# Kernel tuning notes

Measured on AMD Instinct MI355X. Metric: run time of the kernel, lower is better.

Reference implementation:

```python
import jax, jax.numpy as jnp
import numpy as np

N_ATOM, N_TOKEN = 1024, 256
C_S, C_Z, C_ATOM, C_ATOM_PAIR = 384, 128, 128, 16
EPS = 1e-5


def _layer_norm(x, w, b):
    m = jnp.mean(x, axis=-1, keepdims=True)
    v = jnp.mean(jnp.square(x - m), axis=-1, keepdims=True)
    return (x - m) * jax.lax.rsqrt(v + EPS) * w + b


def setup_inputs() -> dict:
    key = jax.random.key(0)
    ks = jax.random.split(key, 12)
    # one-hot atom -> token map (each atom belongs to exactly one token)
    tok_idx = jnp.sort(jax.random.randint(ks[0], (N_ATOM,), 0, N_TOKEN))
    a2t = jax.nn.one_hot(tok_idx, N_TOKEN, dtype=jnp.float32)  # [n_atom, n_token]
    return {
        "atom_to_token_index": a2t,
        "cl": jax.random.normal(ks[1], (N_ATOM, C_ATOM), jnp.float32),
        "plm": jax.random.normal(ks[2], (N_ATOM, N_ATOM, C_ATOM_PAIR), jnp.float32),
        "ql": jax.random.normal(ks[3], (N_ATOM, C_ATOM), jnp.float32),
        "s_trunk": jax.random.normal(ks[4], (N_TOKEN, C_S), jnp.float32),
        "zij": jax.random.normal(ks[5], (N_TOKEN, N_TOKEN, C_Z), jnp.float32),
        "rl": jax.random.normal(ks[6], (N_ATOM, 3), jnp.float32),
        "ln_s_w": jnp.ones((C_S,), jnp.float32),
        "ln_s_b": jnp.zeros((C_S,), jnp.float32),
        "W_s": jax.random.normal(ks[7], (C_S, C_ATOM), jnp.float32) / np.sqrt(C_S),
        "ln_z_w": jnp.ones((C_Z,), jnp.float32),
        "ln_z_b": jnp.zeros((C_Z,), jnp.float32),
        "W_z": jax.random.normal(ks[8], (C_Z, C_ATOM_PAIR), jnp.float32) / np.sqrt(C_Z),
        "W_r": jax.random.normal(ks[9], (3, C_ATOM), jnp.float32) / np.sqrt(3.0),
    }


def reference(atom_to_token_index, cl, plm, ql, s_trunk, zij, rl,
              ln_s_w, ln_s_b, W_s, ln_z_w, ln_z_b, W_z, W_r):
    a2t = atom_to_token_index  # one-hot [n_atom, n_token]
    # cl += Linear_s(LN_s(sum_t s_trunk[t] * a2t[a,t]))  (token->atom broadcast)
    s_atom = jnp.einsum('tc,at->ac', s_trunk, a2t)  # [n_atom, c_s]
    cl = cl + _layer_norm(s_atom, ln_s_w, ln_s_b) @ W_s
    # plm += Linear_z(LN_z(sum_{t,m} zij[t,m] * a2t[a,t] * a2t[b,m]))
    z_at = jnp.einsum('tmc,at->amc', zij, a2t)      # [n_atom, n_token, c_z]
    z_ab = jnp.einsum('amc,bm->abc', z_at, a2t)     # [n_atom, n_atom, c_z]
    plm = plm + _layer_norm(z_ab, ln_z_w, ln_z_b) @ W_z
    # ql += Linear_r(rl)
    ql = ql + rl @ W_r
    return (cl, plm, ql)
```

## Files before the change

### kernel.cpp

```cpp
#include <hip/hip_runtime.h>
#include <hip/hip_bf16.h>

#define NA 1024
#define NT 256
#define CS 384
#define CZ 128
#define CA 128
#define CP 16

typedef __attribute__((ext_vector_type(8))) short short8;
typedef __attribute__((ext_vector_type(4))) float f32x4;

__device__ __forceinline__ float bfu(unsigned short v){ return __uint_as_float(((unsigned)v) << 16); }
__device__ __forceinline__ unsigned short f2bf(float f){
  unsigned u = __float_as_uint(f);
  return (unsigned short)((u + 0x7fffu + ((u >> 16) & 1u)) >> 16);
}
__device__ __forceinline__ unsigned pack2(float lo, float hi){
  return (unsigned)f2bf(lo) | ((unsigned)f2bf(hi) << 16);
}

__device__ __forceinline__ int lbound(const unsigned short* tokL, int key){
  int lo = 0, hi = NA;
  while (lo < hi) { int mid = (lo + hi) >> 1; if ((int)tokL[mid] < key) lo = mid + 1; else hi = mid; }
  return lo;
}

__global__ __launch_bounds__(256) void prep_kernel(
    const float* __restrict__ a2t,
    const float* __restrict__ s_trunk,
    const float* __restrict__ lnsw,
    const float* __restrict__ lnsb,
    const float* __restrict__ Ws,
    unsigned short* __restrict__ tok16,
    unsigned short* __restrict__ ytok)
{
  __shared__ float redS[4], redQ[4];
  __shared__ float lnbuf[CS];
  __shared__ float part[CA];

  const int blk  = blockIdx.x;
  const int tid  = threadIdx.x;
  const int lane = tid & 63;
  const int wv   = tid >> 6;

  if (blk < 256) {
    int a = blk * 4 + wv;
    float4 u = ((const float4*)(a2t + (size_t)a * NT))[lane];
    bool hit = (u.x != 0.f) | (u.y != 0.f) | (u.z != 0.f) | (u.w != 0.f);
    unsigned long long m = __ballot(hit);
    int fl = __ffsll(m) - 1;
    if (lane == fl) {
      int t = lane * 4;
      if (u.x != 0.f)      {  }
      else if (u.y != 0.f) t += 1;
      else if (u.z != 0.f) t += 2;
      else                 t += 3;
      tok16[a] = (unsigned short)t;
    }
  } else {
    int tk = blk - 256;
    float f0 = 0.f, f1 = 0.f;
    if (tid < 192) {
      float2 v = ((const float2*)(s_trunk + (size_t)tk * CS))[tid];
      f0 = v.x; f1 = v.y;
    }
    float s = f0 + f1;
    float q = f0 * f0 + f1 * f1;
    #pragma unroll
    for (int m = 1; m < 64; m <<= 1) { s += __shfl_xor(s, m); q += __shfl_xor(q, m); }
    if (lane == 0) { redS[wv] = s; redQ[wv] = q; }
    __syncthreads();
    if (tid == 0) {
      float S = redS[0] + redS[1] + redS[2] + redS[3];
      float Q = redQ[0] + redQ[1] + redQ[2] + redQ[3];
      float mean = S * (1.f / 384.f);
      float var  = Q * (1.f / 384.f) - mean * mean;
      redS[0] = mean;
      redQ[0] = rsqrtf(var + 1e-5f);
    }
    __syncthreads();
    float mean = redS[0], rstd = redQ[0];
    if (tid < 192) {
      float2 w2 = ((const float2*)lnsw)[tid];
      float2 b2 = ((const float2*)lnsb)[tid];
      lnbuf[2 * tid]     = fmaf((f0 - mean) * rstd, w2.x, b2.x);
      lnbuf[2 * tid + 1] = fmaf((f1 - mean) * rstd, w2.y, b2.y);
    }
    __syncthreads();
    int j = tid & 127, half = tid >> 7;
    float acc = 0.f;
    int c0 = half * 192;
    #pragma unroll 8
    for (int c = c0; c < c0 + 192; ++c)
      acc = fmaf(lnbuf[c], Ws[(size_t)c * CA + j], acc);
    if (half) part[j] = acc;
    __syncthreads();
    if (!half) ytok[(size_t)tk * CA + j] = f2bf(acc + part[j]);
  }
}

__global__ __launch_bounds__(256) void main_kernel(
    const float* __restrict__ cl,
    const float* __restrict__ plm,
    const float* __restrict__ ql,
    const float* __restrict__ rl,
    const float* __restrict__ Wr,
    const float* __restrict__ zij,
    const float* __restrict__ lnzw,
    const float* __restrict__ lnzb,
    const float* __restrict__ Wz,
    const unsigned short* __restrict__ tok16,
    const unsigned short* __restrict__ ytok,
    float* __restrict__ out)
{
  const int blk = blockIdx.x;
  const int tid = threadIdx.x;

  if (blk < 2048) {
    __shared__ unsigned short tokL[NA];
    __shared__ __align__(16) unsigned short ubuf[4 * 16 * 136];
    unsigned short* stage = ubuf;
    float* wlds = (float*)ubuf;

    const int lane = tid & 63;
    const int wv   = tid >> 6;
    const int t    = blk >> 3;
    const int m0   = ((blk >> 1) & 3) << 6;
    const int slot = blk & 1;

    ((uint2*)tokL)[tid] = ((const uint2*)tok16)[tid];
    __syncthreads();

    int s = lbound(tokL, t);
    int e = lbound(tokL, t + 1);
    if (s + slot >= e) return;
    int S = lbound(tokL, m0);
    int E = lbound(tokL, m0 + 64);
    if (S == E) return;

    {
      int r = lane >> 2, q = lane & 3;
      int mrow = m0 + wv * 16 + r;
      const float4* zp = (const float4*)(zij + ((size_t)t * NT + mrow) * CZ + q * 32);
      float x[32];
      float sm = 0.f, ss = 0.f;
      #pragma unroll
      for (int i = 0; i < 8; ++i) {
        float4 v = zp[i];
        x[4 * i]     = v.x; x[4 * i + 1] = v.y;
        x[4 * i + 2] = v.z; x[4 * i + 3] = v.w;
        sm += (v.x + v.y) + (v.z + v.w);
        ss = fmaf(v.x, v.x, ss); ss = fmaf(v.y, v.y, ss);
        ss = fmaf(v.z, v.z, ss); ss = fmaf(v.w, v.w, ss);
      }
      sm += __shfl_xor(sm, 1); sm += __shfl_xor(sm, 2);
      ss += __shfl_xor(ss, 1); ss += __shfl_xor(ss, 2);
      float mean = sm * (1.f / 128.f);
      float var  = ss * (1.f / 128.f) - mean * mean;
      float rstd = rsqrtf(var + 1e-5f);
      unsigned short* st = stage + wv * 2176 + r * 136 + q * 32;
      const float4* lwp = (const float4*)(lnzw + q * 32);
      const float4* lbp = (const float4*)(lnzb + q * 32);
      #pragma unroll
      for (int i = 0; i < 4; ++i) {
        float4 lw0 = lwp[2 * i], lw1 = lwp[2 * i + 1];
        float4 lb0 = lbp[2 * i], lb1 = lbp[2 * i + 1];
        int c = i * 8;
        unsigned o0 = pack2(fmaf((x[c]     - mean) * rstd, lw0.x, lb0.x),
                            fmaf((x[c + 1] - mean) * rstd, lw0.y, lb0.y));
        unsigned o1 = pack2(fmaf((x[c + 2] - mean) * rstd, lw0.z, lb0.z),
                            fmaf((x[c + 3] - mean) * rstd, lw0.w, lb0.w));
        unsigned o2 = pack2(fmaf((x[c + 4] - mean) * rstd, lw1.x, lb1.x),
                            fmaf((x[c + 5] - mean) * rstd, lw1.y, lb1.y));
        unsigned o3 = pack2(fmaf((x[c + 6] - mean) * rstd, lw1.z, lb1.z),
                            fmaf((x[c + 7] - mean) * rstd, lw1.w, lb1.w));
        uint4 ov; ov.x = o0; ov.y = o1; ov.z = o2; ov.w = o3;
        ((uint4*)st)[i] = ov;
      }
      __syncthreads();
      int h = lane >> 4, lm = lane & 15;
      short8 bfrag[4];
      #pragma unroll
      for (int kk = 0; kk < 4; ++kk)
        #pragma unroll
        for (int jj = 0; jj < 8; ++jj)
          bfrag[kk][jj] = (short)f2bf(Wz[(size_t)(kk * 32 + h * 8 + jj) * CP + lm]);
      const unsigned short* sb = stage + wv * 2176;
      short8 af[4];
      #pragma unroll
      for (int kk = 0; kk < 4; ++kk)
        af[kk] = *(const short8*)(sb + lm * 136 + kk * 32 + h * 8);
      f32x4 acc = {0.f, 0.f, 0.f, 0.f};
      #pragma unroll
      for (int kk = 0; kk < 4; ++kk)
        acc = __builtin_amdgcn_mfma_f32_16x16x32_bf16(af[kk], bfrag[kk], acc, 0, 0, 0);
      __syncthreads();
      #pragma unroll
      for (int jj = 0; jj < 4; ++jj)
        wlds[(wv * 16 + h * 4 + jj) * 16 + lm] = acc[jj];
    }
    __syncthreads();

    const float4* plm4 = (const float4*)plm;
    float4* out4 = (float4*)(out + (size_t)NA * CA);
    const int ntask = (E - S) * 4;
    for (int a = s + slot; a < e; a += 2) {
      size_t rowbase = ((size_t)a << 10);
      for (int base = 0; base < ntask; base += 1024) {
        float4 pv[4], wv4[4];
        size_t idx4[4];
        bool act[4];
        #pragma unroll
        for (int j = 0; j < 4; ++j) {
          int task = base + j * 256 + tid;
          act[j] = (task < ntask);
          int tt = act[j] ? task : 0;
          int b = S + (tt >> 2), quar = tt & 3;
          int m = ((int)tokL[b] - m0) & 63;
          idx4[j] = (rowbase + b) * 4 + quar;
          wv4[j] = *(const float4*)(wlds + m * 16 + quar * 4);
          pv[j]  = plm4[idx4[j]];
        }
        #pragma unroll
        for (int j = 0; j < 4; ++j) {
          if (act[j]) {
            float4 ov;
            ov.x = pv[j].x + wv4[j].x; ov.y = pv[j].y + wv4[j].y;
            ov.z = pv[j].z + wv4[j].z; ov.w = pv[j].w + wv4[j].w;
            out4[idx4[j]] = ov;
          }
        }
      }
    }
  } else if (blk < 2560) {
    int idx = (blk - 2048) * 256 + tid;
    int a = idx >> 7, j = idx & 127;
    int ta = (int)tok16[a] & 255;
    out[idx] = cl[idx] + bfu(ytok[(size_t)ta * CA + j]);
  } else {
    int idx = (blk - 2560) * 256 + tid;
    int a = idx >> 7, j = idx & 127;
    float r0 = rl[a * 3 + 0], r1 = rl[a * 3 + 1], r2 = rl[a * 3 + 2];
    float v = ql[idx];
    v = fmaf(r0, Wr[j], v);
    v = fmaf(r1, Wr[CA + j], v);
    v = fmaf(r2, Wr[2 * CA + j], v);
    out[(size_t)NA * CA + (size_t)NA * NA * CP + idx] = v;
  }
}

extern "C" void kernel_launch(void* const* d_in, const int* in_sizes, int n_in,
                              void* d_out, int out_size, void* d_ws, size_t ws_size,
                              hipStream_t stream) {
  const float* a2t     = (const float*)d_in[0];
  const float* cl      = (const float*)d_in[1];
  const float* plm     = (const float*)d_in[2];
  const float* ql      = (const float*)d_in[3];
  const float* s_trunk = (const float*)d_in[4];
  const float* zij     = (const float*)d_in[5];
  const float* rl      = (const float*)d_in[6];
  const float* lnsw    = (const float*)d_in[7];
  const float* lnsb    = (const float*)d_in[8];
  const float* Ws      = (const float*)d_in[9];
  const float* lnzw    = (const float*)d_in[10];
  const float* lnzb    = (const float*)d_in[11];
  const float* Wz      = (const float*)d_in[12];
  const float* Wr      = (const float*)d_in[13];
  float* out = (float*)d_out;

  unsigned short* tok16 = (unsigned short*)d_ws;
  unsigned short* ytok  = (unsigned short*)d_ws + NA;

  prep_kernel<<<512, 256, 0, stream>>>(a2t, s_trunk, lnsw, lnsb, Ws, tok16, ytok);
  main_kernel<<<3072, 256, 0, stream>>>(cl, plm, ql, rl, Wr, zij, lnzw, lnzb, Wz,
                                        tok16, ytok, out);
}
```

Measured before the change: 213.5 us.

## Precompute token-pair LN+projection table, then stream plm with gathered adds

Adds a path that applies LayerNorm and the W_z projection once per token pair (256x256) and stores the result as a bf16 table in workspace. A separate streaming kernel then gathers from that table by atom token indices and adds it to plm, so the LN and matmul are no longer recomputed per atom pair. The old path remains as a fallback when the workspace is too small. The cost is an extra 2 MB table write and read and one more kernel stage, plus bf16 rounding of the projected values.

Result: no change. 210.2 us (-1.5%).

```diff
diff --git a/kernel.cpp b/kernel.cpp
--- a/kernel.cpp
+++ b/kernel.cpp
@@ -10,7 +10,10 @@
 
 typedef __attribute__((ext_vector_type(8))) short short8;
 typedef __attribute__((ext_vector_type(4))) float f32x4;
-
+typedef __attribute__((ext_vector_type(4))) unsigned int u32x4;
+
+__device__ __forceinline__ float bflo(unsigned u){ return __uint_as_float(u << 16); }
+__device__ __forceinline__ float bfhi(unsigned u){ return __uint_as_float(u & 0xffff0000u); }
 __device__ __forceinline__ float bfu(unsigned short v){ return __uint_as_float(((unsigned)v) << 16); }
 __device__ __forceinline__ unsigned short f2bf(float f){
   unsigned u = __float_as_uint(f);
@@ -24,6 +27,201 @@
   int lo = 0, hi = NA;
   while (lo < hi) { int mid = (lo + hi) >> 1; if ((int)tokL[mid] < key) lo = mid + 1; else hi = mid; }
   return lo;
+}
+
+
+__global__ __launch_bounds__(256) void prep_full_kernel(
+    const float* __restrict__ a2t,
+    const float* __restrict__ s_trunk,
+    const float* __restrict__ lnsw,
+    const float* __restrict__ lnsb,
+    const float* __restrict__ Ws,
+    const float* __restrict__ zij,
+    const float* __restrict__ lnzw,
+    const float* __restrict__ lnzb,
+    const float* __restrict__ Wz,
+    unsigned short* __restrict__ tok16,
+    unsigned short* __restrict__ ytok,
+    unsigned short* __restrict__ wtm)
+{
+  __shared__ float redS[4], redQ[4];
+  __shared__ float lnbuf[CS];
+  __shared__ float part[CA];
+  __shared__ __align__(16) unsigned short stage[4 * 16 * 136];
+
+  const int blk  = blockIdx.x;
+  const int tid  = threadIdx.x;
+  const int lane = tid & 63;
+  const int wv   = tid >> 6;
+
+  if (blk < 256) {
+    int a = blk * 4 + wv;
+    float4 u = ((const float4*)(a2t + (size_t)a * NT))[lane];
+    bool hit = (u.x != 0.f) | (u.y != 0.f) | (u.z != 0.f) | (u.w != 0.f);
+    unsigned long long m = __ballot(hit);
+    int fl = __ffsll(m) - 1;
+    if (lane == fl) {
+      int t = lane * 4;
+      if (u.x != 0.f)      { }
+      else if (u.y != 0.f) t += 1;
+      else if (u.z != 0.f) t += 2;
+      else                 t += 3;
+      tok16[a] = (unsigned short)t;
+    }
+  } else if (blk < 512) {
+    int tk = blk - 256;
+    float f0 = 0.f, f1 = 0.f;
+    if (tid < 192) {
+      float2 v = ((const float2*)(s_trunk + (size_t)tk * CS))[tid];
+      f0 = v.x; f1 = v.y;
+    }
+    float s = f0 + f1;
+    float q = f0 * f0 + f1 * f1;
+    #pragma unroll
+    for (int m = 1; m < 64; m <<= 1) { s += __shfl_xor(s, m); q += __shfl_xor(q, m); }
+    if (lane == 0) { redS[wv] = s; redQ[wv] = q; }
+    __syncthreads();
+    if (tid == 0) {
+      float S = redS[0] + redS[1] + redS[2] + redS[3];
+      float Q = redQ[0] + redQ[1] + redQ[2] + redQ[3];
+      float mean = S * (1.f / 384.f);
+      float var  = Q * (1.f / 384.f) - mean * mean;
+      redS[0] = mean;
+      redQ[0] = rsqrtf(var + 1e-5f);
+    }
+    __syncthreads();
+    float mean = redS[0], rstd = redQ[0];
+    if (tid < 192) {
+      float2 w2 = ((const float2*)lnsw)[tid];
+      float2 b2 = ((const float2*)lnsb)[tid];
+      lnbuf[2 * tid]     = fmaf((f0 - mean) * rstd, w2.x, b2.x);
+      lnbuf[2 * tid + 1] = fmaf((f1 - mean) * rstd, w2.y, b2.y);
+    }
+    __syncthreads();
+    int j = tid & 127, half = tid >> 7;
+    float acc = 0.f;
+    int c0 = half * 192;
+    #pragma unroll 8
+    for (int c = c0; c < c0 + 192; ++c)
+      acc = fmaf(lnbuf[c], Ws[(size_t)c * CA + j], acc);
+    if (half) part[j] = acc;
+    __syncthreads();
+    if (!half) ytok[(size_t)tk * CA + j] = f2bf(acc + part[j]);
+  } else {
+    int cb = blk - 512;
+    int r = lane >> 2, q = lane & 3;
+    int rowbase = cb * 64 + wv * 16;
+    const float4* zp = (const float4*)(zij + (size_t)(rowbase + r) * CZ + q * 32);
+    float x[32];
+    float sm = 0.f, ss = 0.f;
+    #pragma unroll
+    for (int i = 0; i < 8; ++i) {
+      float4 v = zp[i];
+      x[4 * i]     = v.x; x[4 * i + 1] = v.y;
+      x[4 * i + 2] = v.z; x[4 * i + 3] = v.w;
+      sm += (v.x + v.y) + (v.z + v.w);
+      ss = fmaf(v.x, v.x, ss); ss = fmaf(v.y, v.y, ss);
+      ss = fmaf(v.z, v.z, ss); ss = fmaf(v.w, v.w, ss);
+    }
+    sm += __shfl_xor(sm, 1); sm += __shfl_xor(sm, 2);
+    ss += __shfl_xor(ss, 1); ss += __shfl_xor(ss, 2);
+    float mean = sm * (1.f / 128.f);
+    float var  = ss * (1.f / 128.f) - mean * mean;
+    float rstd = rsqrtf(var + 1e-5f);
+    unsigned short* st = stage + wv * 2176 + r * 136 + q * 32;
+    const float4* lwp = (const float4*)(lnzw + q * 32);
+    const float4* lbp = (const float4*)(lnzb + q * 32);
+    #pragma unroll
+    for (int i = 0; i < 4; ++i) {
+      float4 lw0 = lwp[2 * i], lw1 = lwp[2 * i + 1];
+      float4 lb0 = lbp[2 * i], lb1 = lbp[2 * i + 1];
+      int c = i * 8;
+      unsigned o0 = pack2(fmaf((x[c]     - mean) * rstd, lw0.x, lb0.x),
+                          fmaf((x[c + 1] - mean) * rstd, lw0.y, lb0.y));
+      unsigned o1 = pack2(fmaf((x[c + 2] - mean) * rstd, lw0.z, lb0.z),
+                          fmaf((x[c + 3] - mean) * rstd, lw0.w, lb0.w));
+      unsigned o2 = pack2(fmaf((x[c + 4] - mean) * rstd, lw1.x, lb1.x),
+                          fmaf((x[c + 5] - mean) * rstd, lw1.y, lb1.y));
+      unsigned o3 = pack2(fmaf((x[c + 6] - mean) * rstd, lw1.z, lb1.z),
+                          fmaf((x[c + 7] - mean) * rstd, lw1.w, lb1.w));
+      uint4 ov; ov.x = o0; ov.y = o1; ov.z = o2; ov.w = o3;
+      ((uint4*)st)[i] = ov;
+    }
+    __syncthreads();
+    int h = lane >> 4, lm = lane & 15;
+    short8 bfrag[4];
+    #pragma unroll
+    for (int kk = 0; kk < 4; ++kk)
+      #pragma unroll
+      for (int jj = 0; jj < 8; ++jj)
+        bfrag[kk][jj] = (short)f2bf(Wz[(size_t)(kk * 32 + h * 8 + jj) * CP + lm]);
+    const unsigned short* sb = stage + wv * 2176;
+    f32x4 acc = {0.f, 0.f, 0.f, 0.f};
+    #pragma unroll
+    for (int kk = 0; kk < 4; ++kk) {
+      short8 af = *(const short8*)(sb + lm * 136 + kk * 32 + h * 8);
+      acc = __builtin_amdgcn_mfma_f32_16x16x32_bf16(af, bfrag[kk], acc, 0, 0, 0);
+    }
+    #pragma unroll
+    for (int jj = 0; jj < 4; ++jj)
+      wtm[(size_t)(rowbase + h * 4 + jj) * CP + lm] = f2bf(acc[jj]);
+  }
+}
+
+__global__ __launch_bounds__(256) void stream_kernel(
+    const float* __restrict__ cl,
+    const float* __restrict__ plm,
+    const float* __restrict__ ql,
+    const float* __restrict__ rl,
+    const float* __restrict__ Wr,
+    const unsigned short* __restrict__ tok16,
+    const unsigned short* __restrict__ ytok,
+    const unsigned short* __restrict__ wtm,
+    float* __restrict__ out)
+{
+  const int blk = blockIdx.x;
+  const int tid = threadIdx.x;
+  if (blk < 4096) {
+    int p = blk * 256 + tid;
+    int a = p >> 10, b = p & 1023;
+    int ta = (int)tok16[a] & 255;
+    int tb = (int)tok16[b] & 255;
+    const u32x4* wp = (const u32x4*)(wtm + (((size_t)ta << 8) + (size_t)tb) * CP);
+    u32x4 w01 = wp[0], w23 = wp[1];
+    const f32x4* pp = (const f32x4*)plm + (size_t)p * 4;
+    f32x4 p0 = __builtin_nontemporal_load(pp);
+    f32x4 p1 = __builtin_nontemporal_load(pp + 1);
+    f32x4 p2 = __builtin_nontemporal_load(pp + 2);
+    f32x4 p3 = __builtin_nontemporal_load(pp + 3);
+    f32x4 o0, o1, o2, o3;
+    o0.x = p0.x + bflo(w01.x); o0.y = p0.y + bfhi(w01.x);
+    o0.z = p0.z + bflo(w01.y); o0.w = p0.w + bfhi(w01.y);
+    o1.x = p1.x + bflo(w01.z); o1.y = p1.y + bfhi(w01.z);
+    o1.z = p1.z + bflo(w01.w); o1.w = p1.w + bfhi(w01.w);
+    o2.x = p2.x + bflo(w23.x); o2.y = p2.y + bfhi(w23.x);
+    o2.z = p2.z + bflo(w23.y); o2.w = p2.w + bfhi(w23.y);
+    o3.x = p3.x + bflo(w23.z); o3.y = p3.y + bfhi(w23.z);
+    o3.z = p3.z + bflo(w23.w); o3.w = p3.w + bfhi(w23.w);
+    f32x4* op = (f32x4*)(out + (size_t)NA * CA) + (size_t)p * 4;
+    __builtin_nontemporal_store(o0, op);
+    __builtin_nontemporal_store(o1, op + 1);
+    __builtin_nontemporal_store(o2, op + 2);
+    __builtin_nontemporal_store(o3, op + 3);
+  } else if (blk < 4608) {
+    int idx = (blk - 4096) * 256 + tid;
+    int a = idx >> 7, j = idx & 127;
+    int ta = (int)tok16[a] & 255;
+    out[idx] = cl[idx] + bfu(ytok[(size_t)ta * CA + j]);
+  } else {
+    int idx = (blk - 4608) * 256 + tid;
+    int a = idx >> 7, j = idx & 127;
+    float r0 = rl[a * 3 + 0], r1 = rl[a * 3 + 1], r2 = rl[a * 3 + 2];
+    float v = ql[idx];
+    v = fmaf(r0, Wr[j], v);
+    v = fmaf(r1, Wr[CA + j], v);
+    v = fmaf(r2, Wr[2 * CA + j], v);
+    out[(size_t)NA * CA + (size_t)NA * NA * CP + idx] = v;
+  }
 }
 
 __global__ __launch_bounds__(256) void prep_kernel(
@@ -52,7 +250,7 @@
     int fl = __ffsll(m) - 1;
     if (lane == fl) {
       int t = lane * 4;
-      if (u.x != 0.f)      {  }
+      if (u.x != 0.f)      { }
       else if (u.y != 0.f) t += 1;
       else if (u.z != 0.f) t += 2;
       else                 t += 3;
@@ -270,9 +468,19 @@
   float* out = (float*)d_out;
 
   unsigned short* tok16 = (unsigned short*)d_ws;
-  unsigned short* ytok  = (unsigned short*)d_ws + NA;
-
-  prep_kernel<<<512, 256, 0, stream>>>(a2t, s_trunk, lnsw, lnsb, Ws, tok16, ytok);
-  main_kernel<<<3072, 256, 0, stream>>>(cl, plm, ql, rl, Wr, zij, lnzw, lnzb, Wz,
-                                        tok16, ytok, out);
-}
+  unsigned short* ytok  = (unsigned short*)((char*)d_ws + 2048);
+  unsigned short* wtm   = (unsigned short*)((char*)d_ws + 67584);
+  const size_t WS_NEEDED_A = 67584 + (size_t)NT * NT * CP * 2;
+
+  if (ws_size >= WS_NEEDED_A) {
+    prep_full_kernel<<<1536, 256, 0, stream>>>(a2t, s_trunk, lnsw, lnsb, Ws,
+                                               zij, lnzw, lnzb, Wz,
+                                               tok16, ytok, wtm);
+    stream_kernel<<<5120, 256, 0, stream>>>(cl, plm, ql, rl, Wr,
+                                            tok16, ytok, wtm, out);
+  } else {
+    prep_kernel<<<512, 256, 0, stream>>>(a2t, s_trunk, lnsw, lnsb, Ws, tok16, ytok);
+    main_kernel<<<3072, 256, 0, stream>>>(cl, plm, ql, rl, Wr, zij, lnzw, lnzb, Wz,
+                                          tok16, ytok, out);
+  }
+}
```
